# Optimization experiments

Hardware: AMD Instinct MI355X
Metric: run time of the kernel (lower is better)

## Reference

```python
import jax, jax.numpy as jnp
import numpy as np

B, C, H, W = 4, 128, 96, 96
E = 4
C8 = C // 8


def _conv1x1(w, b, x):
    # w: [out, in], x: [b, in, H, W]
    return jnp.einsum('oi,bihw->bohw', w, x) + b[None, :, None, None]


def _bilinear_zeros(x, gx, gy):
    # x: [b, C, h, w]; gx, gy: [b, H2, W2] normalized coords in [-1, 1]
    # align_corners=True, padding_mode='zeros' (matches F.grid_sample)
    b, c, h, w = x.shape
    ix = (gx + 1.0) * 0.5 * (w - 1)
    iy = (gy + 1.0) * 0.5 * (h - 1)
    ix0 = jnp.floor(ix)
    iy0 = jnp.floor(iy)
    tx = ix - ix0
    ty = iy - iy0
    ix0 = ix0.astype(jnp.int32)
    iy0 = iy0.astype(jnp.int32)

    def gather(yy, xx):
        valid = ((xx >= 0) & (xx < w) & (yy >= 0) & (yy < h)).astype(x.dtype)
        xc = jnp.clip(xx, 0, w - 1)
        yc = jnp.clip(yy, 0, h - 1)
        vals = jax.vmap(lambda xb, y, xi: xb[:, y, xi])(x, yc, xc)  # [b,C,H2,W2]
        return vals * valid[:, None]

    w00 = ((1 - tx) * (1 - ty))[:, None]
    w01 = (tx * (1 - ty))[:, None]
    w10 = ((1 - tx) * ty)[:, None]
    w11 = (tx * ty)[:, None]
    return (gather(iy0, ix0) * w00 + gather(iy0, ix0 + 1) * w01
            + gather(iy0 + 1, ix0) * w10 + gather(iy0 + 1, ix0 + 1) * w11)


def setup_inputs() -> dict:
    key = jax.random.key(0)
    ks = jax.random.split(key, 12)
    s = 0.05
    return {
        'x': jax.random.normal(ks[0], (B, C, H, W), jnp.float32),
        'weight_compress': jax.random.normal(ks[1], (E, C8, C), jnp.float32) * s,
        'weight_expand': jax.random.normal(ks[2], (E, C, C8), jnp.float32) * s,
        'body_w1': jax.random.normal(ks[3], (64, 3), jnp.float32) * s,
        'body_b1': jax.random.normal(ks[4], (64,), jnp.float32) * s,
        'body_w2': jax.random.normal(ks[5], (64, 64), jnp.float32) * s,
        'body_b2': jax.random.normal(ks[6], (64,), jnp.float32) * s,
        'rout_w': jax.random.normal(ks[7], (E, 64), jnp.float32) * s,
        'rout_b': jax.random.normal(ks[8], (E,), jnp.float32) * s,
        'off_w': jax.random.normal(ks[9], (2, 64), jnp.float32) * s,
        'off_b': jax.random.normal(ks[10], (2,), jnp.float32) * s,
        'scale': 2,
    }


def reference(x, weight_compress, weight_expand, body_w1, body_b1,
              body_w2, body_b2, rout_w, rout_b, off_w, off_b, scale):
    b, c, h, w = x.shape
    sc = float(scale)
    H2 = round(h * sc)
    W2 = round(w * sc)

    # fractional sub-pixel coordinates (meta-upsample positional encoding)
    ch = (jnp.arange(H2, dtype=jnp.float32) + 0.5) / sc
    ch = ch - jnp.floor(ch + 0.001) - 0.5  # [H2]
    cw = (jnp.arange(W2, dtype=jnp.float32) + 0.5) / sc
    cw = cw - jnp.floor(cw + 0.001) - 0.5  # [W2]
    inp = jnp.stack([
        jnp.full((H2, W2), 1.0 / sc, jnp.float32),
        jnp.broadcast_to(ch[:, None], (H2, W2)),
        jnp.broadcast_to(cw[None, :], (H2, W2)),
    ], axis=0)[None]  # [1, 3, H2, W2]

    emb = jax.nn.relu(_conv1x1(body_w1, body_b1, inp))
    emb = jax.nn.relu(_conv1x1(body_w2, body_b2, emb))
    offset = _conv1x1(off_w, off_b, emb)                      # [1, 2, H2, W2]
    routing = jax.nn.sigmoid(_conv1x1(rout_w, rout_b, emb))   # [1, E, H2, W2]
    r = routing[0].transpose(1, 2, 0)                         # [H2, W2, E]

    # base sampling grid, align_corners=True normalization + learned offset
    gx = ((jnp.arange(W2, dtype=jnp.float32) + 0.5) / sc - 0.5) * 2.0 / (w - 1) - 1.0
    gy = ((jnp.arange(H2, dtype=jnp.float32) + 0.5) / sc - 0.5) * 2.0 / (h - 1) - 1.0
    gx = gx[None, None, :] + offset[:, 0] * 2.0 / (w - 1)     # [1, H2, W2]
    gy = gy[None, :, None] + offset[:, 1] * 2.0 / (h - 1)
    gx = jnp.broadcast_to(gx, (b, H2, W2))
    gy = jnp.broadcast_to(gy, (b, H2, W2))

    fea0 = _bilinear_zeros(x, gx, gy)          # [b, C, H2, W2]
    fea = fea0.transpose(0, 2, 3, 1)           # [b, H2, W2, C]

    # per-pixel routed 1x1 convs: compress (C->C/8) then expand (C/8->C)
    comp = jnp.einsum('bhwc,hwe,eoc->bhwo', fea, r, weight_compress)
    out = jnp.einsum('bhwo,hwe,eco->bhwc', comp, r, weight_expand)
    return out.transpose(0, 3, 1, 2) + fea0
```

## Files before the change

kernel.cpp:

```cpp
#include <hip/hip_runtime.h>
#include <math.h>

#define Bn 4
#define Cc 128
#define Hh 96
#define Ww 96
#define H2c 192
#define W2c 192
#define HW (Hh*Ww)
#define HW2 (H2c*W2c)

#define WC_OFF 0
#define WE_OFF (4*2048)
#define TAP_OFF (8*2048)
#define M_OFF  16640

typedef float  f32x4  __attribute__((ext_vector_type(4)));
typedef short  s16x8  __attribute__((ext_vector_type(8)));

__device__ __forceinline__ unsigned f2bf(float f) {
    unsigned u = __float_as_uint(f);
    return (u + 0x7FFFu + ((u >> 16) & 1u)) >> 16;
}

__device__ __forceinline__ void gload_lds16(const float* g, float* l) {
    __builtin_amdgcn_global_load_lds(
        (const __attribute__((address_space(1))) unsigned int*)g,
        (__attribute__((address_space(3))) unsigned int*)l,
        16, 0, 0);
}

__global__ __launch_bounds__(256) void k1_mix(
    const float* __restrict__ wcomp, const float* __restrict__ wexp,
    const float* __restrict__ bw1, const float* __restrict__ bb1,
    const float* __restrict__ bw2, const float* __restrict__ bb2,
    const float* __restrict__ rw,  const float* __restrict__ rb,
    const float* __restrict__ ow,  const float* __restrict__ ob,
    float* __restrict__ ws)
{
    __shared__ float e1[64], e2[64], rr[4], of[2];
    const int tid   = threadIdx.x;
    const int cls   = blockIdx.x >> 4;
    const int chunk = blockIdx.x & 15;
    const float chv = (cls & 2) ? 0.25f : -0.25f;
    const float cwv = (cls & 1) ? 0.25f : -0.25f;

    if (tid < 64) {
        float h = bw1[tid*3+0]*0.5f + bw1[tid*3+1]*chv + bw1[tid*3+2]*cwv + bb1[tid];
        e1[tid] = fmaxf(h, 0.f);
    }
    __syncthreads();
    if (tid < 64) {
        float s = bb2[tid];
        for (int i = 0; i < 64; ++i) s += bw2[tid*64+i]*e1[i];
        e2[tid] = fmaxf(s, 0.f);
    }
    __syncthreads();
    if (tid < 6) {
        if (tid < 4) {
            float s = rb[tid];
            for (int i = 0; i < 64; ++i) s += rw[tid*64+i]*e2[i];
            rr[tid] = 1.f/(1.f+expf(-s));
        } else {
            const int d = tid - 4;
            float s = ob[d];
            for (int i = 0; i < 64; ++i) s += ow[d*64+i]*e2[i];
            of[d] = s;
        }
    }
    __syncthreads();
    const float r0 = rr[0], r1 = rr[1], r2 = rr[2], r3 = rr[3];

    if (tid < 128) {
        const int idx = chunk*128 + tid;
        const int o = idx >> 7, c = idx & 127;
        const float v = r0*wcomp[idx] + r1*wcomp[2048+idx]
                      + r2*wcomp[4096+idx] + r3*wcomp[6144+idx];
        ws[WC_OFF + cls*2048 + c*16 + o] = v;
    } else {
        const int idx = chunk*128 + (tid - 128);
        ws[WE_OFF + cls*2048 + idx] =
            r0*wexp[idx] + r1*wexp[2048+idx] + r2*wexp[4096+idx] + r3*wexp[6144+idx];
    }
    if (chunk == 0 && tid == 0) {
        const float fx = cwv + of[0];
        const float fy = chv + of[1];
        const float Dx = floorf(fx), Dy = floorf(fy);
        ws[TAP_OFF + cls*4 + 0] = fx - Dx;
        ws[TAP_OFF + cls*4 + 1] = fy - Dy;
        ws[TAP_OFF + cls*4 + 2] = Dx;
        ws[TAP_OFF + cls*4 + 3] = Dy;
    }
}

__global__ __launch_bounds__(256) void k1b_fold(
    const float* __restrict__ wsr, unsigned short* __restrict__ Mw)
{
    const int t   = blockIdx.x*256 + threadIdx.x;
    const int cls = t >> 12;
    const int rem = t & 4095;
    const int co  = rem >> 5;
    const int ci0 = (rem & 31) * 4;
    const float* we = wsr + WE_OFF + cls*2048 + co*16;

    float m[4];
    #pragma unroll
    for (int q = 0; q < 4; ++q) {
        const float* wc = wsr + WC_OFF + cls*2048 + (ci0+q)*16;
        float s = 0.f;
        #pragma unroll
        for (int o = 0; o < 16; ++o) s += we[o]*wc[o];
        if (co == ci0 + q) s += 1.f;
        m[q] = s;
    }
    uint2 v;
    v.x = f2bf(m[0]) | (f2bf(m[1]) << 16);
    v.y = f2bf(m[2]) | (f2bf(m[3]) << 16);
    *reinterpret_cast<uint2*>(Mw + (size_t)cls*16384 + co*128 + ci0) = v;
}

__device__ __forceinline__ void remap_axis(int c0, int last, float w0, float w1,
                                           int& base, float& a0, float& a1)
{
    base = min(max(c0, 0), last - 1);
    if (c0 >= 0 && c0 < last) { a0 = w0;  a1 = w1;  }
    else if (c0 == -1)        { a0 = w1;  a1 = 0.f; }
    else if (c0 == last)      { a0 = 0.f; a1 = w0;  }
    else                      { a0 = 0.f; a1 = 0.f; }
}

__global__ __launch_bounds__(256) void k2_mfma(
    const float* __restrict__ x, const float* __restrict__ wsr,
    const unsigned short* __restrict__ Mw, float* __restrict__ out)
{
    __shared__ __align__(16) unsigned short lF[64*128];
    __shared__ __align__(16) float lWin[4*2*512];

    const int tid = threadIdx.x;
    const int xl  = tid & 63;
    const int grp = tid >> 6;

    const int n  = blockIdx.x;
    const int w  = (n & 7)*288 + (n >> 3);
    const int b  = w / 576;
    const int rr = w % 576;
    const int yg = rr / 3;
    const int xt = rr % 3;
    const int ygp = yg & 1;
    const int j   = yg >> 1;
    const int i0  = xt*32;
    const int clsE = ygp << 1;

    const int px = xl & 1;
    const int i  = i0 + (xl >> 1);
    const int cls = clsE | px;

    const float txE = wsr[TAP_OFF + clsE*4 + 0], txO = wsr[TAP_OFF + (clsE|1)*4 + 0];
    const float tyE = wsr[TAP_OFF + clsE*4 + 1], tyO = wsr[TAP_OFF + (clsE|1)*4 + 1];
    const int   DxE = (int)wsr[TAP_OFF + clsE*4 + 2], DxO = (int)wsr[TAP_OFF + (clsE|1)*4 + 2];
    const int   DyE = (int)wsr[TAP_OFF + clsE*4 + 3], DyO = (int)wsr[TAP_OFF + (clsE|1)*4 + 3];
    const float tx = px ? txO : txE;
    const float ty = px ? tyO : tyE;
    const int   Dx = px ? DxO : DxE;
    const int   Dy = px ? DyO : DyE;

    int basex, basey; float ax0, ax1, ay0, ay1;
    remap_axis(i + Dx, Ww - 1, 1.f - tx, tx, basex, ax0, ax1);
    remap_axis(j + Dy, Hh - 1, 1.f - ty, ty, basey, ay0, ay1);
    const float w00 = ay0*ax0, w01 = ay0*ax1, w10 = ay1*ax0, w11 = ay1*ax1;

    const int minDx = min(DxE, DxO), minDy = min(DyE, DyO);
    const int cs0 = min(max((i0 + minDx) & ~3, 0), Ww - 40);
    const int jDc = min(j + minDy, Hh - 2);
    const int ro0 = (basey - jDc)*40 + (basex - cs0);
    const int ro1 = ro0 + 40;

    const int sl = xl & 31;
    const int s2 = min(sl, 29);
    const int lr = s2 / 10, lq = s2 - lr*10;
    const int lrow = min(max(jDc + lr, 0), Hh - 1);
    const float* gsrc = x + (size_t)b*Cc*HW + (size_t)lrow*Ww + cs0 + 4*lq;
    const int chsub = xl >> 5;

    float* winw = lWin + grp*1024;
    const int slot = px*32 + (xl >> 1);

#define ISSUE(q) { \
    _Pragma("unroll") \
    for (int p = 0; p < 2; ++p) \
        gload_lds16(gsrc + (size_t)(grp*32 + (q)*4 + p*2 + chsub)*HW, \
                    winw + ((q)&1)*512 + p*256); }

    ISSUE(0)
    ISSUE(1)
    #pragma unroll
    for (int q = 0; q < 8; ++q) {
        if (q < 7) asm volatile("s_waitcnt vmcnt(2)" ::: "memory");
        else       asm volatile("s_waitcnt vmcnt(0)" ::: "memory");
        __builtin_amdgcn_sched_barrier(0);
        {
            const float* wb = winw + (q&1)*512;
            float f[4];
            #pragma unroll
            for (int u = 0; u < 4; ++u) {
                const float* wc = wb + (u>>1)*256 + (u&1)*128;
                f[u] = w00*wc[ro0] + w01*wc[ro0+1] + w10*wc[ro1] + w11*wc[ro1+1];
            }
            uint2 v;
            v.x = f2bf(f[0]) | (f2bf(f[1]) << 16);
            v.y = f2bf(f[2]) | (f2bf(f[3]) << 16);
            const int c = grp*32 + q*4;
            int byte = slot*256 + c*2;
            byte ^= (slot & 7) << 4;
            *reinterpret_cast<uint2*>(reinterpret_cast<char*>(lF) + byte) = v;
        }
        if (q < 6) {
            asm volatile("s_waitcnt lgkmcnt(0)" ::: "memory");
            __builtin_amdgcn_sched_barrier(0);
            ISSUE(q+2)
        }
    }
#undef ISSUE
    __syncthreads();

    const int lo = xl & 15, hi = xl >> 4;
    f32x4 acc[2][4];
    #pragma unroll
    for (int t = 0; t < 2; ++t)
        #pragma unroll
        for (int nn = 0; nn < 4; ++nn) acc[t][nn] = (f32x4){0.f, 0.f, 0.f, 0.f};

    #pragma unroll
    for (int ph = 0; ph < 2; ++ph) {
        const unsigned short* Mc = Mw + (size_t)(clsE | ph)*16384;
        s16x8 mf[2][4];
        #pragma unroll
        for (int t = 0; t < 2; ++t)
            #pragma unroll
            for (int kk = 0; kk < 4; ++kk)
                mf[t][kk] = *reinterpret_cast<const s16x8*>(
                    Mc + (32*grp + 16*t + lo)*128 + kk*32 + hi*8);
        #pragma unroll
        for (int kk = 0; kk < 4; ++kk) {
            #pragma unroll
            for (int q2 = 0; q2 < 2; ++q2) {
                const int nn = ph*2 + q2;
                const int row = nn*16 + lo;
                int byte = row*256 + kk*64 + hi*16;
                byte ^= (row & 7) << 4;
                const s16x8 af = *reinterpret_cast<const s16x8*>(
                    reinterpret_cast<const char*>(lF) + byte);
                acc[0][nn] = __builtin_amdgcn_mfma_f32_16x16x32_bf16(af, mf[0][kk], acc[0][nn], 0, 0, 0);
                acc[1][nn] = __builtin_amdgcn_mfma_f32_16x16x32_bf16(af, mf[1][kk], acc[1][nn], 0, 0, 0);
            }
        }
    }

    #pragma unroll
    for (int t = 0; t < 2; ++t) {
        const int ch = 32*grp + 16*t + lo;
        float* rowp = out + ((size_t)(b*Cc + ch)*H2c + yg)*W2c;
        #pragma unroll
        for (int p = 0; p < 2; ++p) {
            const f32x4 e = acc[t][p], o = acc[t][p+2];
            const f32x4 v0 = {e[0], o[0], e[1], o[1]};
            const f32x4 v1 = {e[2], o[2], e[3], o[3]};
            float* op = rowp + 2*i0 + p*32 + hi*8;
            *reinterpret_cast<f32x4*>(op)     = v0;
            *reinterpret_cast<f32x4*>(op + 4) = v1;
        }
    }
}

extern "C" void kernel_launch(void* const* d_in, const int* in_sizes, int n_in,
                              void* d_out, int out_size, void* d_ws, size_t ws_size,
                              hipStream_t stream) {
    const float* x     = (const float*)d_in[0];
    const float* wcomp = (const float*)d_in[1];
    const float* wexp  = (const float*)d_in[2];
    const float* bw1   = (const float*)d_in[3];
    const float* bb1   = (const float*)d_in[4];
    const float* bw2   = (const float*)d_in[5];
    const float* bb2   = (const float*)d_in[6];
    const float* rw    = (const float*)d_in[7];
    const float* rb    = (const float*)d_in[8];
    const float* ow    = (const float*)d_in[9];
    const float* ob    = (const float*)d_in[10];
    float* out = (float*)d_out;
    float* ws  = (float*)d_ws;
    unsigned short* Mw = (unsigned short*)(ws + M_OFF);

    k1_mix<<<64, 256, 0, stream>>>(wcomp, wexp, bw1, bb1, bw2, bb2, rw, rb, ow, ob, ws);
    k1b_fold<<<64, 256, 0, stream>>>(ws, Mw);
    k2_mfma<<<2304, 256, 0, stream>>>(x, ws, Mw, out);
}
```

Before: 51.98 us.

## Fuse weight mixing into fold kernel and stage output stores through LDS

Merges the routing-weight mix kernel and the fold kernel into one prep kernel that mixes expert weights on the fly while building the folded bf16 matrix. This removes one launch and the intermediate workspace round trip. The MFMA kernel now shares one LDS buffer between the input window and feature tiles. It writes accumulators to a swizzled LDS tile so each block emits fully contiguous 64-float row segments with 16-byte stores, replacing scattered 32-byte chunks. In exchange it adds two block barriers and redundant weight-mixing arithmetic in the prep kernel.

After: 58.33 us. +12.2%, slower.

```diff
diff --git a/kernel.cpp b/kernel.cpp
--- a/kernel.cpp
+++ b/kernel.cpp
@@ -10,10 +10,8 @@
 #define HW (Hh*Ww)
 #define HW2 (H2c*W2c)
 
-#define WC_OFF 0
-#define WE_OFF (4*2048)
-#define TAP_OFF (8*2048)
-#define M_OFF  16640
+#define TAP_OFF 0
+#define M_OFF 16
 
 typedef float  f32x4  __attribute__((ext_vector_type(4)));
 typedef short  s16x8  __attribute__((ext_vector_type(8)));
@@ -26,19 +24,18 @@
 __device__ __forceinline__ void gload_lds16(const float* g, float* l) {
     __builtin_amdgcn_global_load_lds(
         (const __attribute__((address_space(1))) unsigned int*)g,
-        (__attribute__((address_space(3))) unsigned int*)l,
-        16, 0, 0);
-}
-
-__global__ __launch_bounds__(256) void k1_mix(
+        (__attribute__((address_space(3))) unsigned int*)l, 16, 0, 0);
+}
+
+__global__ __launch_bounds__(256) void k1_prep(
     const float* __restrict__ wcomp, const float* __restrict__ wexp,
     const float* __restrict__ bw1, const float* __restrict__ bb1,
     const float* __restrict__ bw2, const float* __restrict__ bb2,
     const float* __restrict__ rw,  const float* __restrict__ rb,
     const float* __restrict__ ow,  const float* __restrict__ ob,
-    float* __restrict__ ws)
+    float* __restrict__ ws, unsigned short* __restrict__ Mw)
 {
-    __shared__ float e1[64], e2[64], rr[4], of[2];
+    __shared__ float e1[64], e2[64], rr4[4], of2[2];
     const int tid   = threadIdx.x;
     const int cls   = blockIdx.x >> 4;
     const int chunk = blockIdx.x & 15;
@@ -60,57 +57,47 @@
         if (tid < 4) {
             float s = rb[tid];
             for (int i = 0; i < 64; ++i) s += rw[tid*64+i]*e2[i];
-            rr[tid] = 1.f/(1.f+expf(-s));
+            rr4[tid] = 1.f/(1.f+expf(-s));
         } else {
             const int d = tid - 4;
             float s = ob[d];
             for (int i = 0; i < 64; ++i) s += ow[d*64+i]*e2[i];
-            of[d] = s;
-        }
-    }
-    __syncthreads();
-    const float r0 = rr[0], r1 = rr[1], r2 = rr[2], r3 = rr[3];
-
-    if (tid < 128) {
-        const int idx = chunk*128 + tid;
-        const int o = idx >> 7, c = idx & 127;
-        const float v = r0*wcomp[idx] + r1*wcomp[2048+idx]
-                      + r2*wcomp[4096+idx] + r3*wcomp[6144+idx];
-        ws[WC_OFF + cls*2048 + c*16 + o] = v;
-    } else {
-        const int idx = chunk*128 + (tid - 128);
-        ws[WE_OFF + cls*2048 + idx] =
-            r0*wexp[idx] + r1*wexp[2048+idx] + r2*wexp[4096+idx] + r3*wexp[6144+idx];
-    }
+            of2[d] = s;
+        }
+    }
+    __syncthreads();
+    const float r0 = rr4[0], r1 = rr4[1], r2 = rr4[2], r3 = rr4[3];
+
     if (chunk == 0 && tid == 0) {
-        const float fx = cwv + of[0];
-        const float fy = chv + of[1];
+        const float fx = cwv + of2[0];
+        const float fy = chv + of2[1];
         const float Dx = floorf(fx), Dy = floorf(fy);
         ws[TAP_OFF + cls*4 + 0] = fx - Dx;
         ws[TAP_OFF + cls*4 + 1] = fy - Dy;
         ws[TAP_OFF + cls*4 + 2] = Dx;
         ws[TAP_OFF + cls*4 + 3] = Dy;
     }
-}
-
-__global__ __launch_bounds__(256) void k1b_fold(
-    const float* __restrict__ wsr, unsigned short* __restrict__ Mw)
-{
-    const int t   = blockIdx.x*256 + threadIdx.x;
-    const int cls = t >> 12;
-    const int rem = t & 4095;
-    const int co  = rem >> 5;
-    const int ci0 = (rem & 31) * 4;
-    const float* we = wsr + WE_OFF + cls*2048 + co*16;
-
+
+    const int co  = chunk*8 + (tid >> 5);
+    const int ci0 = (tid & 31) * 4;
+    const float* weB = wexp + co*16;
+    float wem[16];
+    #pragma unroll
+    for (int o = 0; o < 16; ++o)
+        wem[o] = r0*weB[o] + r1*weB[2048+o] + r2*weB[4096+o] + r3*weB[6144+o];
     float m[4];
     #pragma unroll
     for (int q = 0; q < 4; ++q) {
-        const float* wc = wsr + WC_OFF + cls*2048 + (ci0+q)*16;
+        const int ci = ci0 + q;
+        const float* wcB = wcomp + ci;
         float s = 0.f;
         #pragma unroll
-        for (int o = 0; o < 16; ++o) s += we[o]*wc[o];
-        if (co == ci0 + q) s += 1.f;
+        for (int o = 0; o < 16; ++o) {
+            const float wcm = r0*wcB[o*128]        + r1*wcB[2048 + o*128]
+                            + r2*wcB[4096 + o*128] + r3*wcB[6144 + o*128];
+            s += wem[o]*wcm;
+        }
+        if (co == ci) s += 1.f;
         m[q] = s;
     }
     uint2 v;
@@ -133,8 +120,9 @@
     const float* __restrict__ x, const float* __restrict__ wsr,
     const unsigned short* __restrict__ Mw, float* __restrict__ out)
 {
-    __shared__ __align__(16) unsigned short lF[64*128];
-    __shared__ __align__(16) float lWin[4*2*512];
+    __shared__ __align__(16) char ldsu[32768];
+    float*          lWin = reinterpret_cast<float*>(ldsu);
+    unsigned short* lF   = reinterpret_cast<unsigned short*>(ldsu + 16384);
 
     const int tid = threadIdx.x;
     const int xl  = tid & 63;
@@ -153,7 +141,6 @@
 
     const int px = xl & 1;
     const int i  = i0 + (xl >> 1);
-    const int cls = clsE | px;
 
     const float txE = wsr[TAP_OFF + clsE*4 + 0], txO = wsr[TAP_OFF + (clsE|1)*4 + 0];
     const float tyE = wsr[TAP_OFF + clsE*4 + 1], tyO = wsr[TAP_OFF + (clsE|1)*4 + 1];
@@ -175,8 +162,7 @@
     const int ro0 = (basey - jDc)*40 + (basex - cs0);
     const int ro1 = ro0 + 40;
 
-    const int sl = xl & 31;
-    const int s2 = min(sl, 29);
+    const int sl = xl & 31, s2 = min(sl, 29);
     const int lr = s2 / 10, lq = s2 - lr*10;
     const int lrow = min(max(jDc + lr, 0), Hh - 1);
     const float* gsrc = x + (size_t)b*Cc*HW + (size_t)lrow*Ww + cs0 + 4*lq;
@@ -256,19 +242,34 @@
         }
     }
 
+    __syncthreads();
+    float* lO = reinterpret_cast<float*>(ldsu);
+
     #pragma unroll
     for (int t = 0; t < 2; ++t) {
         const int ch = 32*grp + 16*t + lo;
-        float* rowp = out + ((size_t)(b*Cc + ch)*H2c + yg)*W2c;
-        #pragma unroll
-        for (int p = 0; p < 2; ++p) {
-            const f32x4 e = acc[t][p], o = acc[t][p+2];
-            const f32x4 v0 = {e[0], o[0], e[1], o[1]};
-            const f32x4 v1 = {e[2], o[2], e[3], o[3]};
-            float* op = rowp + 2*i0 + p*32 + hi*8;
-            *reinterpret_cast<f32x4*>(op)     = v0;
-            *reinterpret_cast<f32x4*>(op + 4) = v1;
-        }
+        const int sw = (ch & 7) << 2;
+        #pragma unroll
+        for (int nn = 0; nn < 4; ++nn) {
+            #pragma unroll
+            for (int r = 0; r < 4; ++r) {
+                const int slot2 = nn*16 + hi*4 + r;
+                const int xgl = (nn < 2) ? (2*slot2) : (2*(slot2 - 32) + 1);
+                lO[ch*64 + (xgl ^ sw)] = acc[t][nn][r];
+            }
+        }
+    }
+    __syncthreads();
+
+    #pragma unroll
+    for (int k = 0; k < 8; ++k) {
+        const int F  = tid*4 + k*1024;
+        const int ch = F >> 6;
+        const int m4 = F & 63;
+        const int sw = (ch & 7) << 2;
+        const f32x4 v = *reinterpret_cast<const f32x4*>(lO + ch*64 + (m4 ^ sw));
+        float* op = out + ((size_t)(b*Cc + ch)*H2c + yg)*W2c + xt*64 + m4;
+        *reinterpret_cast<f32x4*>(op) = v;
     }
 }
 
@@ -290,7 +291,7 @@
     float* ws  = (float*)d_ws;
     unsigned short* Mw = (unsigned short*)(ws + M_OFF);
 
-    k1_mix<<<64, 256, 0, stream>>>(wcomp, wexp, bw1, bb1, bw2, bb2, rw, rb, ow, ob, ws);
-    k1b_fold<<<64, 256, 0, stream>>>(ws, Mw);
+    k1_prep<<<64, 256, 0, stream>>>(wcomp, wexp, bw1, bb1, bw2, bb2,
+                                    rw, rb, ow, ob, ws, Mw);
     k2_mfma<<<2304, 256, 0, stream>>>(x, ws, Mw, out);
 }
```
